# Kernel optimization log

Hardware: AMD Instinct MI355X
Metric: run time of the kernel (lower is better)

Reference implementation:

```python
import jax, jax.numpy as jnp
import numpy as np

B, S = 128, 400
EMB, ENC, DEC = 128, 1024, 300
VOCAB, MAX_OOV = 50000, 50


def setup_inputs() -> dict:
    key = jax.random.key(0)
    ks = jax.random.split(key, 16)
    s = 0.05
    return {
        "embedded": jax.random.normal(ks[0], (B, EMB), jnp.float32),
        "enc_output": jax.random.normal(ks[1], (B, S, ENC), jnp.float32),
        "h1": jax.random.normal(ks[2], (B, DEC), jnp.float32),
        "pad_mask": jnp.zeros((B, S), jnp.bool_),
        "max_n_oov": MAX_OOV,
        "source_WORD_encoding_extended": jax.random.randint(ks[3], (B, S), 0, VOCAB + MAX_OOV),
        # parameters
        "W_attn1": jax.random.normal(ks[4], (ENC, DEC), jnp.float32) * s,
        "W_attn2": jax.random.normal(ks[5], (ENC, DEC), jnp.float32) * s,
        "W_ih": jax.random.normal(ks[6], (3 * DEC, EMB + ENC), jnp.float32) * s,
        "W_hh": jax.random.normal(ks[7], (3 * DEC, DEC), jnp.float32) * s,
        "b_ih": jax.random.normal(ks[8], (3 * DEC,), jnp.float32) * s,
        "b_hh": jax.random.normal(ks[9], (3 * DEC,), jnp.float32) * s,
        "W_out": jax.random.normal(ks[10], (VOCAB, ENC + DEC), jnp.float32) * s,
        "b_out": jax.random.normal(ks[11], (VOCAB,), jnp.float32) * s,
        "W_p": jax.random.normal(ks[12], (1, ENC + DEC), jnp.float32) * s,
        "b_p": jax.random.normal(ks[13], (1,), jnp.float32) * s,
    }


def _additive_attn(h, enc_output, W, pad_mask):
    # h: [B, DEC], enc_output: [B, S, ENC], W: [ENC, DEC]
    e = jnp.einsum('bse,ed->bsd', enc_output, W)
    scores = jnp.einsum('bd,bsd->bs', h, e)
    scores = jnp.where(pad_mask, -jnp.inf, scores)
    return jax.nn.softmax(scores, axis=1)  # [B, S]


def _gru_cell(x, h, W_ih, W_hh, b_ih, b_hh):
    gx = x @ W_ih.T + b_ih  # [B, 3*DEC]
    gh = h @ W_hh.T + b_hh
    xr, xz, xn = jnp.split(gx, 3, axis=1)
    hr, hz, hn = jnp.split(gh, 3, axis=1)
    r = jax.nn.sigmoid(xr + hr)
    z = jax.nn.sigmoid(xz + hz)
    n = jnp.tanh(xn + r * hn)
    return (1.0 - z) * n + z * h


def reference(embedded, enc_output, h1, pad_mask, max_n_oov,
              source_WORD_encoding_extended, W_attn1, W_attn2,
              W_ih, W_hh, b_ih, b_hh, W_out, b_out, W_p, b_p):
    a = _additive_attn(h1, enc_output, W_attn1, pad_mask)
    weighted = jnp.einsum('bs,bse->be', a, enc_output)
    rnn_input = jnp.concatenate([embedded, weighted], axis=1)
    h_new = _gru_cell(rnn_input, h1, W_ih, W_hh, b_ih, b_hh)

    a2 = _additive_attn(h_new, enc_output, W_attn2, pad_mask)
    weighted2 = jnp.einsum('bs,bse->be', a2, enc_output)
    hw = jnp.concatenate([h_new, weighted2], axis=1)  # [B, DEC+ENC]

    p_vocab = jax.nn.softmax(hw @ W_out.T + b_out, axis=1)  # [B, VOCAB]
    p_gen = jax.nn.sigmoid(hw @ W_p.T + b_p)  # [B, 1]

    bsz = p_vocab.shape[0]
    ext_zeros = jnp.zeros((bsz, max_n_oov), p_vocab.dtype)
    p_out = p_gen * jnp.concatenate([p_vocab, ext_zeros], axis=1)
    rows = jnp.arange(bsz)[:, None]
    p_out = p_out.at[rows, source_WORD_encoding_extended].add((1.0 - p_gen) * a2)
    return p_out, h_new
```

## Files before the change

### kernel.cpp

```cpp
#include <hip/hip_runtime.h>
#include <stdint.h>

constexpr int B_     = 128;
constexpr int S_     = 400;
constexpr int EMB_   = 128;
constexpr int ENC_   = 1024;
constexpr int DEC_   = 300;
constexpr int VOCAB_ = 50000;
constexpr int OOV_   = 50;
constexpr int OUTW_  = VOCAB_ + OOV_;
constexpr int KHW_   = ENC_ + DEC_;
constexpr int KHWP_  = 1344;
constexpr int G3_    = 3 * DEC_;
constexpr int KIN_   = EMB_ + ENC_;
constexpr int CHK_   = 192;
constexpr int ALDS_STRIDE_ = 200;
constexpr int PSTRIDE_ = 1028;

typedef __attribute__((ext_vector_type(4))) float f32x4;
typedef __attribute__((ext_vector_type(8))) short short8;

__device__ __forceinline__ float dot4(float4 a, float4 b) {
  return a.x * b.x + a.y * b.y + a.z * b.z + a.w * b.w;
}

__device__ __forceinline__ short f2bf(float f) {
  uint32_t u = __builtin_bit_cast(uint32_t, f);
  u += 0x7fffu + ((u >> 16) & 1u);
  return (short)(u >> 16);
}

__global__ __launch_bounds__(256) void k_compute_v(const float* __restrict__ W,
                                                   const float* __restrict__ h,
                                                   float* __restrict__ v) {
  int b = blockIdx.x;
  __shared__ __align__(16) float hs[DEC_];
  for (int d = threadIdx.x; d < DEC_; d += 256) hs[d] = h[b * DEC_ + d];
  __syncthreads();
  for (int e = threadIdx.x; e < ENC_; e += 256) {
    const float4* w4 = (const float4*)(W + (size_t)e * DEC_);
    const float4* h4 = (const float4*)hs;
    float acc = 0.f;
    #pragma unroll 5
    for (int d = 0; d < DEC_ / 4; ++d) acc += dot4(w4[d], h4[d]);
    v[b * ENC_ + e] = acc;
  }
}

__global__ __launch_bounds__(256) void k_attn_pass(const float* __restrict__ enc,
                                                   const float* __restrict__ v,
                                                   float* __restrict__ scores,
                                                   float* __restrict__ part, int nsplit) {
  int b = blockIdx.x, split = blockIdx.y;
  int wave = threadIdx.x >> 6, lane = threadIdx.x & 63;
  float4 vr[4];
  #pragma unroll
  for (int c = 0; c < 4; ++c) vr[c] = *(const float4*)(v + b * ENC_ + c * 256 + lane * 4);
  float m = -INFINITY, l = 0.f;
  float4 wa[4];
  #pragma unroll
  for (int c = 0; c < 4; ++c) wa[c] = make_float4(0.f, 0.f, 0.f, 0.f);
  int rows = S_ / nsplit, s0 = split * rows;
  for (int s = s0 + wave; s < s0 + rows; s += 4) {
    const float* er = enc + ((size_t)b * S_ + s) * ENC_;
    float4 e4[4];
    #pragma unroll
    for (int c = 0; c < 4; ++c) e4[c] = *(const float4*)(er + c * 256 + lane * 4);
    float p = 0.f;
    #pragma unroll
    for (int c = 0; c < 4; ++c) p += dot4(e4[c], vr[c]);
    #pragma unroll
    for (int off = 32; off; off >>= 1) p += __shfl_xor(p, off);
    if (lane == 0) scores[b * S_ + s] = p;
    float nm = fmaxf(m, p);
    float sc = __expf(m - nm);
    float pe = __expf(p - nm);
    l = l * sc + pe;
    #pragma unroll
    for (int c = 0; c < 4; ++c) {
      wa[c].x = wa[c].x * sc + pe * e4[c].x;
      wa[c].y = wa[c].y * sc + pe * e4[c].y;
      wa[c].z = wa[c].z * sc + pe * e4[c].z;
      wa[c].w = wa[c].w * sc + pe * e4[c].w;
    }
    m = nm;
  }
  float* pp = part + ((size_t)b * (nsplit * 4) + split * 4 + wave) * PSTRIDE_;
  #pragma unroll
  for (int c = 0; c < 4; ++c) *(float4*)(pp + c * 256 + lane * 4) = wa[c];
  if (lane == 0) { pp[1024] = m; pp[1025] = l; }
}

__global__ __launch_bounds__(256) void k_attn_merge(const float* __restrict__ part, int P,
                                                    float* __restrict__ wout, int wstride,
                                                    int woff, float* __restrict__ ml) {
  int b = blockIdx.x, tid = threadIdx.x;
  const float* pb = part + (size_t)b * P * PSTRIDE_;
  __shared__ float scl[32];
  __shared__ float Ls;
  if (tid == 0) {
    float M = -INFINITY;
    for (int p = 0; p < P; ++p) M = fmaxf(M, pb[p * PSTRIDE_ + 1024]);
    float L = 0.f;
    for (int p = 0; p < P; ++p) {
      float lp = pb[p * PSTRIDE_ + 1025];
      float e = (lp > 0.f) ? __expf(pb[p * PSTRIDE_ + 1024] - M) : 0.f;
      scl[p] = e;
      L += lp * e;
    }
    Ls = L;
    if (ml) { ml[b * 2] = M; ml[b * 2 + 1] = L; }
  }
  __syncthreads();
  float invL = 1.f / Ls;
  for (int e = tid; e < ENC_; e += 256) {
    float acc = 0.f;
    for (int p = 0; p < P; ++p) acc += scl[p] * pb[p * PSTRIDE_ + e];
    wout[(size_t)b * wstride + woff + e] = acc * invL;
  }
}

__global__ __launch_bounds__(256) void k_gates(const float* __restrict__ emb,
                                               const float* __restrict__ wgt,
                                               const float* __restrict__ h1,
                                               const float* __restrict__ W_ih,
                                               const float* __restrict__ W_hh,
                                               const float* __restrict__ b_ih,
                                               const float* __restrict__ b_hh,
                                               float* __restrict__ gx, float* __restrict__ gh) {
  int idx = blockIdx.x * 256 + threadIdx.x;
  int b = idx & (B_ - 1);
  int g = idx >> 7;
  if (g >= G3_) return;
  const float4* wr = (const float4*)(W_ih + (size_t)g * KIN_);
  const float4* xe = (const float4*)(emb + b * EMB_);
  const float4* xw = (const float4*)(wgt + b * ENC_);
  float accx = b_ih[g];
  #pragma unroll 8
  for (int k = 0; k < EMB_ / 4; ++k) accx += dot4(wr[k], xe[k]);
  #pragma unroll 8
  for (int k = 0; k < ENC_ / 4; ++k) accx += dot4(wr[EMB_ / 4 + k], xw[k]);
  const float4* wh = (const float4*)(W_hh + (size_t)g * DEC_);
  const float4* xh = (const float4*)(h1 + b * DEC_);
  float acch = b_hh[g];
  #pragma unroll 5
  for (int k = 0; k < DEC_ / 4; ++k) acch += dot4(wh[k], xh[k]);
  gx[g * B_ + b] = accx;
  gh[g * B_ + b] = acch;
}

__global__ __launch_bounds__(256) void k_gru_combine(const float* __restrict__ gx,
                                                     const float* __restrict__ gh,
                                                     const float* __restrict__ h1,
                                                     float* __restrict__ hn,
                                                     float* __restrict__ hw,
                                                     float* __restrict__ outh) {
  int j = blockIdx.x * 256 + threadIdx.x;
  int b = blockIdx.y;
  if (j >= DEC_) return;
  float xr = gx[j * B_ + b], xz = gx[(j + DEC_) * B_ + b], xn = gx[(j + 2 * DEC_) * B_ + b];
  float hr = gh[j * B_ + b], hz = gh[(j + DEC_) * B_ + b], hnn = gh[(j + 2 * DEC_) * B_ + b];
  float r = 1.f / (1.f + __expf(-(xr + hr)));
  float z = 1.f / (1.f + __expf(-(xz + hz)));
  float n = tanhf(xn + r * hnn);
  float h = (1.f - z) * n + z * h1[b * DEC_ + j];
  hn[b * DEC_ + j] = h;
  hw[(size_t)b * KHW_ + j] = h;
  outh[b * DEC_ + j] = h;
}

__global__ __launch_bounds__(256) void k_pgen_cast(const float* __restrict__ hw,
                                                   const float* __restrict__ W_p,
                                                   const float* __restrict__ b_p,
                                                   float* __restrict__ pg,
                                                   short* __restrict__ hwb) {
  int b = blockIdx.x, t = threadIdx.x;
  __shared__ float red[256];
  const float* row = hw + (size_t)b * KHW_;
  float acc = 0.f;
  for (int k = t; k < KHW_; k += 256) acc += row[k] * W_p[k];
  red[t] = acc;
  __syncthreads();
  for (int st = 128; st > 0; st >>= 1) {
    if (t < st) red[t] += red[t + st];
    __syncthreads();
  }
  if (t == 0) pg[b] = 1.f / (1.f + __expf(-(red[0] + b_p[0])));
  for (int k = t; k < KHWP_; k += 256)
    hwb[(size_t)b * KHWP_ + k] = (k < KHW_) ? f2bf(row[k]) : (short)0;
}

__global__ __launch_bounds__(256) void k_outproj(const short* __restrict__ A,
                                                 const float* __restrict__ Wo,
                                                 const float* __restrict__ bo,
                                                 float* __restrict__ out) {
  __shared__ __align__(16) short A_lds[B_ * ALDS_STRIDE_];
  int tid = threadIdx.x;
  int wave = tid >> 6, lane = tid & 63;
  int r16 = lane & 15, kg = lane >> 4;
  int vcol = blockIdx.x * 64 + wave * 16 + r16;
  int vload = vcol < VOCAB_ ? vcol : VOCAB_ - 1;
  const float* brow = Wo + (size_t)vload * KHW_ + kg * 8;
  f32x4 acc[8];
  #pragma unroll
  for (int mi = 0; mi < 8; ++mi) acc[mi] = (f32x4){0.f, 0.f, 0.f, 0.f};

  short8 ar[12];
  float4 br[2][12];
  float  tl[8];

  #pragma unroll
  for (int i = 0; i < 12; ++i) {
    int g = tid + i * 256, row = g / 24, c8 = g % 24;
    ar[i] = *(const short8*)(A + (size_t)row * KHWP_ + c8 * 8);
  }
  #pragma unroll
  for (int s = 0; s < 6; ++s) {
    br[0][2 * s]     = *(const float4*)(brow + s * 32);
    br[0][2 * s + 1] = *(const float4*)(brow + s * 32 + 4);
  }

  #pragma unroll
  for (int c = 0; c < 7; ++c) {
    __syncthreads();
    #pragma unroll
    for (int i = 0; i < 12; ++i) {
      int g = tid + i * 256, row = g / 24, c8 = g % 24;
      *(short8*)(&A_lds[row * ALDS_STRIDE_ + c8 * 8]) = ar[i];
    }
    if (c < 6) {
      #pragma unroll
      for (int i = 0; i < 12; ++i) {
        int g = tid + i * 256, row = g / 24, c8 = g % 24;
        ar[i] = *(const short8*)(A + (size_t)row * KHWP_ + (c + 1) * CHK_ + c8 * 8);
      }
      if (c + 1 < 6) {
        #pragma unroll
        for (int s = 0; s < 6; ++s) {
          br[(c + 1) & 1][2 * s]     = *(const float4*)(brow + (c + 1) * CHK_ + s * 32);
          br[(c + 1) & 1][2 * s + 1] = *(const float4*)(brow + (c + 1) * CHK_ + s * 32 + 4);
        }
      } else {
        #pragma unroll
        for (int s = 0; s < 5; ++s) {
          br[0][2 * s]     = *(const float4*)(brow + 6 * CHK_ + s * 32);
          br[0][2 * s + 1] = *(const float4*)(brow + 6 * CHK_ + s * 32 + 4);
        }
        #pragma unroll
        for (int j = 0; j < 8; ++j)
          tl[j] = (kg * 8 + j < KHW_ - 1312) ? brow[1312 + j] : 0.f;
      }
    }
    __syncthreads();
    #pragma unroll
    for (int s = 0; s < 6; ++s) {
      short8 bf;
      if (c == 6 && s == 5) {
        #pragma unroll
        for (int j = 0; j < 8; ++j) bf[j] = f2bf(tl[j]);
      } else {
        float4 b0 = br[c & 1][2 * s], b1 = br[c & 1][2 * s + 1];
        bf[0] = f2bf(b0.x); bf[1] = f2bf(b0.y); bf[2] = f2bf(b0.z); bf[3] = f2bf(b0.w);
        bf[4] = f2bf(b1.x); bf[5] = f2bf(b1.y); bf[6] = f2bf(b1.z); bf[7] = f2bf(b1.w);
      }
      #pragma unroll
      for (int mi = 0; mi < 8; ++mi) {
        short8 af = *(const short8*)(&A_lds[(mi * 16 + r16) * ALDS_STRIDE_ + s * 32 + kg * 8]);
        acc[mi] = __builtin_amdgcn_mfma_f32_16x16x32_bf16(af, bf, acc[mi], 0, 0, 0);
      }
    }
  }

  if (vcol < VOCAB_) {
    float bias = bo[vcol];
    #pragma unroll
    for (int mi = 0; mi < 8; ++mi) {
      #pragma unroll
      for (int j = 0; j < 4; ++j) {
        out[(size_t)(mi * 16 + kg * 4 + j) * OUTW_ + vcol] = acc[mi][j] + bias;
      }
    }
  }
}

__global__ __launch_bounds__(256) void k_vocab_softmax(float* __restrict__ out,
                                                       const float* __restrict__ pg,
                                                       const int* __restrict__ src,
                                                       const float* __restrict__ scores,
                                                       const float* __restrict__ ml2) {
  int b = blockIdx.x, t = threadIdx.x;
  float* row = out + (size_t)b * OUTW_;
  __shared__ float red[256];
  float mx = -INFINITY;
  for (int v = t; v < VOCAB_; v += 256) mx = fmaxf(mx, row[v]);
  red[t] = mx;
  __syncthreads();
  for (int st = 128; st > 0; st >>= 1) {
    if (t < st) red[t] = fmaxf(red[t], red[t + st]);
    __syncthreads();
  }
  float M = red[0];
  __syncthreads();
  float sm = 0.f;
  for (int v = t; v < VOCAB_; v += 256) sm += __expf(row[v] - M);
  red[t] = sm;
  __syncthreads();
  for (int st = 128; st > 0; st >>= 1) {
    if (t < st) red[t] += red[t + st];
    __syncthreads();
  }
  float p = pg[b];
  float scale = p / red[0];
  for (int v = t; v < OUTW_; v += 256) {
    row[v] = (v < VOCAB_) ? scale * __expf(row[v] - M) : 0.f;
  }
  __syncthreads();
  float M2 = ml2[b * 2], L2 = ml2[b * 2 + 1];
  float q = (1.f - p) / L2;
  for (int s = t; s < S_; s += 256) {
    float val = q * __expf(scores[b * S_ + s] - M2);
    atomicAdd(row + src[b * S_ + s], val);
  }
}

extern "C" void kernel_launch(void* const* d_in, const int* in_sizes, int n_in,
                              void* d_out, int out_size, void* d_ws, size_t ws_size,
                              hipStream_t stream) {
  const float* embedded = (const float*)d_in[0];
  const float* enc      = (const float*)d_in[1];
  const float* h1       = (const float*)d_in[2];
  const int*   src      = (const int*)d_in[5];
  const float* W1       = (const float*)d_in[6];
  const float* W2       = (const float*)d_in[7];
  const float* W_ih     = (const float*)d_in[8];
  const float* W_hh     = (const float*)d_in[9];
  const float* b_ih     = (const float*)d_in[10];
  const float* b_hh     = (const float*)d_in[11];
  const float* W_out    = (const float*)d_in[12];
  const float* b_out    = (const float*)d_in[13];
  const float* W_p      = (const float*)d_in[14];
  const float* b_p      = (const float*)d_in[15];
  float* out = (float*)d_out;
  float* ws  = (float*)d_ws;

  size_t off = 0;
  float* v_ws    = ws + off; off += (size_t)B_ * ENC_;
  float* w1_ws   = ws + off; off += (size_t)B_ * ENC_;
  float* gx_ws   = ws + off; off += (size_t)G3_ * B_;
  float* gh_ws   = ws + off; off += (size_t)G3_ * B_;
  float* hn_ws   = ws + off; off += (size_t)B_ * DEC_;
  float* hw_ws   = ws + off; off += (size_t)B_ * KHW_;
  float* sc_ws   = ws + off; off += (size_t)B_ * S_;
  float* ml2_ws  = ws + off; off += 256;
  float* pg_ws   = ws + off; off += 128;
  short* hwb_ws  = (short*)(ws + off); off += (size_t)B_ * KHWP_ / 2;
  float* part_ws = ws + off;

  int NS = 4;
  if ((off + (size_t)B_ * NS * 4 * PSTRIDE_) * 4 > ws_size) NS = 1;

  k_compute_v<<<B_, 256, 0, stream>>>(W1, h1, v_ws);
  k_attn_pass<<<dim3(B_, NS), 256, 0, stream>>>(enc, v_ws, sc_ws, part_ws, NS);
  k_attn_merge<<<B_, 256, 0, stream>>>(part_ws, NS * 4, w1_ws, ENC_, 0, nullptr);
  k_gates<<<(G3_ * B_) / 256, 256, 0, stream>>>(embedded, w1_ws, h1, W_ih, W_hh, b_ih, b_hh,
                                                gx_ws, gh_ws);
  k_gru_combine<<<dim3(2, B_), 256, 0, stream>>>(gx_ws, gh_ws, h1, hn_ws, hw_ws,
                                                 out + (size_t)B_ * OUTW_);
  k_compute_v<<<B_, 256, 0, stream>>>(W2, hn_ws, v_ws);
  k_attn_pass<<<dim3(B_, NS), 256, 0, stream>>>(enc, v_ws, sc_ws, part_ws, NS);
  k_attn_merge<<<B_, 256, 0, stream>>>(part_ws, NS * 4, hw_ws, KHW_, DEC_, ml2_ws);
  k_pgen_cast<<<B_, 256, 0, stream>>>(hw_ws, W_p, b_p, pg_ws, hwb_ws);
  k_outproj<<<(VOCAB_ + 63) / 64, 256, 0, stream>>>(hwb_ws, W_out, b_out, out);
  k_vocab_softmax<<<B_, 256, 0, stream>>>(out, pg_ws, src, sc_ws, ml2_ws);
}
```

Before: 477.5 us.

## Fuse vocab softmax stats into outproj, fold pgen into merges, unroll attention

The output projection now computes per-tile row max and sum-exp partials, and a new split kernel merges them and normalises the vocab logits in a single pass. This replaces the old three-pass per-row softmax that ran on only one block per batch row. The p_gen dot product and the bf16 cast are folded into the GRU combine and the second attention merge, which removes the k_pgen_cast kernel and the fp32 hw buffer. The attention pass now processes two rows per iteration and uses up to 8 splits for more parallelism, at the cost of extra workspace and an atomic accumulation for p_gen.

```diff
diff --git a/kernel.cpp b/kernel.cpp
--- a/kernel.cpp
+++ b/kernel.cpp
@@ -16,6 +16,7 @@
 constexpr int CHK_   = 192;
 constexpr int ALDS_STRIDE_ = 200;
 constexpr int PSTRIDE_ = 1028;
+constexpr int NTILE_ = 782;
 
 typedef __attribute__((ext_vector_type(4))) float f32x4;
 typedef __attribute__((ext_vector_type(8))) short short8;
@@ -60,8 +61,41 @@
   float4 wa[4];
   #pragma unroll
   for (int c = 0; c < 4; ++c) wa[c] = make_float4(0.f, 0.f, 0.f, 0.f);
-  int rows = S_ / nsplit, s0 = split * rows;
-  for (int s = s0 + wave; s < s0 + rows; s += 4) {
+  int rows = S_ / nsplit, s0 = split * rows, s_end = s0 + rows;
+  int s = s0 + wave;
+  for (; s + 4 < s_end; s += 8) {
+    const float* era = enc + ((size_t)b * S_ + s) * ENC_;
+    const float* erb = enc + ((size_t)b * S_ + s + 4) * ENC_;
+    float4 e4a[4], e4b[4];
+    #pragma unroll
+    for (int c = 0; c < 4; ++c) {
+      e4a[c] = *(const float4*)(era + c * 256 + lane * 4);
+      e4b[c] = *(const float4*)(erb + c * 256 + lane * 4);
+    }
+    float pa = 0.f, pb = 0.f;
+    #pragma unroll
+    for (int c = 0; c < 4; ++c) { pa += dot4(e4a[c], vr[c]); pb += dot4(e4b[c], vr[c]); }
+    #pragma unroll
+    for (int off = 32; off; off >>= 1) {
+      pa += __shfl_xor(pa, off);
+      pb += __shfl_xor(pb, off);
+    }
+    if (lane == 0) { scores[b * S_ + s] = pa; scores[b * S_ + s + 4] = pb; }
+    float nm = fmaxf(m, fmaxf(pa, pb));
+    float sc = __expf(m - nm);
+    float ea = __expf(pa - nm);
+    float eb = __expf(pb - nm);
+    l = l * sc + ea + eb;
+    #pragma unroll
+    for (int c = 0; c < 4; ++c) {
+      wa[c].x = wa[c].x * sc + ea * e4a[c].x + eb * e4b[c].x;
+      wa[c].y = wa[c].y * sc + ea * e4a[c].y + eb * e4b[c].y;
+      wa[c].z = wa[c].z * sc + ea * e4a[c].z + eb * e4b[c].z;
+      wa[c].w = wa[c].w * sc + ea * e4a[c].w + eb * e4b[c].w;
+    }
+    m = nm;
+  }
+  if (s < s_end) {
     const float* er = enc + ((size_t)b * S_ + s) * ENC_;
     float4 e4[4];
     #pragma unroll
@@ -73,8 +107,7 @@
     for (int off = 32; off; off >>= 1) p += __shfl_xor(p, off);
     if (lane == 0) scores[b * S_ + s] = p;
     float nm = fmaxf(m, p);
-    float sc = __expf(m - nm);
-    float pe = __expf(p - nm);
+    float sc = __expf(m - nm), pe = __expf(p - nm);
     l = l * sc + pe;
     #pragma unroll
     for (int c = 0; c < 4; ++c) {
@@ -91,9 +124,8 @@
   if (lane == 0) { pp[1024] = m; pp[1025] = l; }
 }
 
-__global__ __launch_bounds__(256) void k_attn_merge(const float* __restrict__ part, int P,
-                                                    float* __restrict__ wout, int wstride,
-                                                    int woff, float* __restrict__ ml) {
+__global__ __launch_bounds__(256) void k_attn_merge1(const float* __restrict__ part, int P,
+                                                     float* __restrict__ wout) {
   int b = blockIdx.x, tid = threadIdx.x;
   const float* pb = part + (size_t)b * P * PSTRIDE_;
   __shared__ float scl[32];
@@ -109,15 +141,59 @@
       L += lp * e;
     }
     Ls = L;
-    if (ml) { ml[b * 2] = M; ml[b * 2 + 1] = L; }
   }
   __syncthreads();
   float invL = 1.f / Ls;
   for (int e = tid; e < ENC_; e += 256) {
     float acc = 0.f;
     for (int p = 0; p < P; ++p) acc += scl[p] * pb[p * PSTRIDE_ + e];
-    wout[(size_t)b * wstride + woff + e] = acc * invL;
-  }
+    wout[(size_t)b * ENC_ + e] = acc * invL;
+  }
+}
+
+__global__ __launch_bounds__(256) void k_attn_merge2(const float* __restrict__ part, int P,
+                                                     short* __restrict__ hwb,
+                                                     float* __restrict__ ml,
+                                                     const float* __restrict__ W_p,
+                                                     const float* __restrict__ b_p,
+                                                     const float* __restrict__ pg_acc,
+                                                     float* __restrict__ pg) {
+  int b = blockIdx.x, tid = threadIdx.x;
+  const float* pb = part + (size_t)b * P * PSTRIDE_;
+  __shared__ float scl[32];
+  __shared__ float Ls;
+  __shared__ float red[256];
+  if (tid == 0) {
+    float M = -INFINITY;
+    for (int p = 0; p < P; ++p) M = fmaxf(M, pb[p * PSTRIDE_ + 1024]);
+    float L = 0.f;
+    for (int p = 0; p < P; ++p) {
+      float lp = pb[p * PSTRIDE_ + 1025];
+      float e = (lp > 0.f) ? __expf(pb[p * PSTRIDE_ + 1024] - M) : 0.f;
+      scl[p] = e;
+      L += lp * e;
+    }
+    Ls = L;
+    ml[b * 2] = M; ml[b * 2 + 1] = L;
+  }
+  __syncthreads();
+  float invL = 1.f / Ls;
+  float pacc = 0.f;
+  for (int e = tid; e < ENC_; e += 256) {
+    float acc = 0.f;
+    for (int p = 0; p < P; ++p) acc += scl[p] * pb[p * PSTRIDE_ + e];
+    float w = acc * invL;
+    hwb[(size_t)b * KHWP_ + DEC_ + e] = f2bf(w);
+    pacc += w * W_p[DEC_ + e];
+  }
+  if (tid < KHWP_ - KHW_) hwb[(size_t)b * KHWP_ + KHW_ + tid] = 0;
+  red[tid] = pacc;
+  __syncthreads();
+  for (int st = 128; st > 0; st >>= 1) {
+    if (tid < st) red[tid] += red[tid + st];
+    __syncthreads();
+  }
+  if (tid == 0) pg[b] = 1.f / (1.f + __expf(-(red[0] + pg_acc[b] + b_p[0])));
 }
 
 __global__ __launch_bounds__(256) void k_gates(const float* __restrict__ emb,
@@ -127,8 +203,10 @@
                                                const float* __restrict__ W_hh,
                                                const float* __restrict__ b_ih,
                                                const float* __restrict__ b_hh,
-                                               float* __restrict__ gx, float* __restrict__ gh) {
+                                               float* __restrict__ gx, float* __restrict__ gh,
+                                               float* __restrict__ pg_acc) {
   int idx = blockIdx.x * 256 + threadIdx.x;
+  if (idx < B_) pg_acc[idx] = 0.f;
   int b = idx & (B_ - 1);
   int g = idx >> 7;
   if (g >= G3_) return;
@@ -153,48 +231,42 @@
                                                      const float* __restrict__ gh,
                                                      const float* __restrict__ h1,
                                                      float* __restrict__ hn,
-                                                     float* __restrict__ hw,
-                                                     float* __restrict__ outh) {
+                                                     short* __restrict__ hwb,
+                                                     float* __restrict__ outh,
+                                                     const float* __restrict__ W_p,
+                                                     float* __restrict__ pg_acc) {
   int j = blockIdx.x * 256 + threadIdx.x;
   int b = blockIdx.y;
-  if (j >= DEC_) return;
-  float xr = gx[j * B_ + b], xz = gx[(j + DEC_) * B_ + b], xn = gx[(j + 2 * DEC_) * B_ + b];
-  float hr = gh[j * B_ + b], hz = gh[(j + DEC_) * B_ + b], hnn = gh[(j + 2 * DEC_) * B_ + b];
-  float r = 1.f / (1.f + __expf(-(xr + hr)));
-  float z = 1.f / (1.f + __expf(-(xz + hz)));
-  float n = tanhf(xn + r * hnn);
-  float h = (1.f - z) * n + z * h1[b * DEC_ + j];
-  hn[b * DEC_ + j] = h;
-  hw[(size_t)b * KHW_ + j] = h;
-  outh[b * DEC_ + j] = h;
-}
-
-__global__ __launch_bounds__(256) void k_pgen_cast(const float* __restrict__ hw,
-                                                   const float* __restrict__ W_p,
-                                                   const float* __restrict__ b_p,
-                                                   float* __restrict__ pg,
-                                                   short* __restrict__ hwb) {
-  int b = blockIdx.x, t = threadIdx.x;
   __shared__ float red[256];
-  const float* row = hw + (size_t)b * KHW_;
-  float acc = 0.f;
-  for (int k = t; k < KHW_; k += 256) acc += row[k] * W_p[k];
-  red[t] = acc;
+  float pp = 0.f;
+  if (j < DEC_) {
+    float xr = gx[j * B_ + b], xz = gx[(j + DEC_) * B_ + b], xn = gx[(j + 2 * DEC_) * B_ + b];
+    float hr = gh[j * B_ + b], hz = gh[(j + DEC_) * B_ + b], hnn = gh[(j + 2 * DEC_) * B_ + b];
+    float r = 1.f / (1.f + __expf(-(xr + hr)));
+    float z = 1.f / (1.f + __expf(-(xz + hz)));
+    float n = tanhf(xn + r * hnn);
+    float h = (1.f - z) * n + z * h1[b * DEC_ + j];
+    hn[b * DEC_ + j] = h;
+    hwb[(size_t)b * KHWP_ + j] = f2bf(h);
+    outh[b * DEC_ + j] = h;
+    pp = h * W_p[j];
+  }
+  red[threadIdx.x] = pp;
   __syncthreads();
   for (int st = 128; st > 0; st >>= 1) {
-    if (t < st) red[t] += red[t + st];
+    if (threadIdx.x < st) red[threadIdx.x] += red[threadIdx.x + st];
     __syncthreads();
   }
-  if (t == 0) pg[b] = 1.f / (1.f + __expf(-(red[0] + b_p[0])));
-  for (int k = t; k < KHWP_; k += 256)
-    hwb[(size_t)b * KHWP_ + k] = (k < KHW_) ? f2bf(row[k]) : (short)0;
+  if (threadIdx.x == 0) atomicAdd(pg_acc + b, red[0]);
 }
 
 __global__ __launch_bounds__(256) void k_outproj(const short* __restrict__ A,
                                                  const float* __restrict__ Wo,
                                                  const float* __restrict__ bo,
-                                                 float* __restrict__ out) {
+                                                 float* __restrict__ out,
+                                                 float* __restrict__ pml) {
   __shared__ __align__(16) short A_lds[B_ * ALDS_STRIDE_];
+  __shared__ float wml[4][B_][2];
   int tid = threadIdx.x;
   int wave = tid >> 6, lane = tid & 63;
   int r16 = lane & 15, kg = lane >> 4;
@@ -271,52 +343,88 @@
     }
   }
 
-  if (vcol < VOCAB_) {
-    float bias = bo[vcol];
-    #pragma unroll
-    for (int mi = 0; mi < 8; ++mi) {
+  bool valid = vcol < VOCAB_;
+  float biasv = bo[vload];
+  #pragma unroll
+  for (int mi = 0; mi < 8; ++mi) {
+    #pragma unroll
+    for (int j = 0; j < 4; ++j) {
+      float lv = valid ? acc[mi][j] + biasv : -INFINITY;
+      if (valid) out[(size_t)(mi * 16 + kg * 4 + j) * OUTW_ + vcol] = lv;
+      float mr = lv;
       #pragma unroll
-      for (int j = 0; j < 4; ++j) {
-        out[(size_t)(mi * 16 + kg * 4 + j) * OUTW_ + vcol] = acc[mi][j] + bias;
+      for (int msk = 1; msk < 16; msk <<= 1) mr = fmaxf(mr, __shfl_xor(mr, msk));
+      float se = valid ? __expf(lv - mr) : 0.f;
+      #pragma unroll
+      for (int msk = 1; msk < 16; msk <<= 1) se += __shfl_xor(se, msk);
+      if (r16 == 0) {
+        wml[wave][mi * 16 + kg * 4 + j][0] = mr;
+        wml[wave][mi * 16 + kg * 4 + j][1] = se;
       }
     }
   }
-}
-
-__global__ __launch_bounds__(256) void k_vocab_softmax(float* __restrict__ out,
-                                                       const float* __restrict__ pg,
-                                                       const int* __restrict__ src,
-                                                       const float* __restrict__ scores,
-                                                       const float* __restrict__ ml2) {
+  __syncthreads();
+  if (tid < B_) {
+    float M = -INFINITY;
+    #pragma unroll
+    for (int w = 0; w < 4; ++w) M = fmaxf(M, wml[w][tid][0]);
+    float L = 0.f;
+    #pragma unroll
+    for (int w = 0; w < 4; ++w) {
+      float lw = wml[w][tid][1];
+      if (lw > 0.f) L += lw * __expf(wml[w][tid][0] - M);
+    }
+    pml[((size_t)blockIdx.x * B_ + tid) * 2]     = M;
+    pml[((size_t)blockIdx.x * B_ + tid) * 2 + 1] = L;
+  }
+}
+
+__global__ __launch_bounds__(256) void k_vfinal(float* __restrict__ out,
+                                                const float* __restrict__ pml,
+                                                const float* __restrict__ pg,
+                                                float* __restrict__ mlv) {
+  int bq = blockIdx.x, b = blockIdx.y, t = threadIdx.x;
+  __shared__ float rm[256], rl[256];
+  float lm = -INFINITY, ll = 0.f;
+  for (int tile = t; tile < NTILE_; tile += 256) {
+    float m = pml[((size_t)tile * B_ + b) * 2];
+    float l = pml[((size_t)tile * B_ + b) * 2 + 1];
+    float M = fmaxf(lm, m);
+    float nl = 0.f;
+    if (ll > 0.f) nl += ll * __expf(lm - M);
+    if (l > 0.f) nl += l * __expf(m - M);
+    lm = M; ll = nl;
+  }
+  rm[t] = lm; rl[t] = ll;
+  __syncthreads();
+  for (int st = 128; st > 0; st >>= 1) {
+    if (t < st) {
+      float m1 = rm[t], l1 = rl[t], m2 = rm[t + st], l2 = rl[t + st];
+      float M = fmaxf(m1, m2);
+      float L = (l1 > 0.f ? l1 * __expf(m1 - M) : 0.f) + (l2 > 0.f ? l2 * __expf(m2 - M) : 0.f);
+      rm[t] = M; rl[t] = L;
+    }
+    __syncthreads();
+  }
+  float M = rm[0], L = rl[0];
+  float scale = pg[b] / L;
+  float* row = out + (size_t)b * OUTW_;
+  int lo = bq * 12513;
+  int hi = min(lo + 12513, OUTW_);
+  for (int v = lo + t; v < hi; v += 256)
+    row[v] = (v < VOCAB_) ? scale * __expf(row[v] - M) : 0.f;
+  if (bq == 0 && t == 0) { mlv[b * 2] = M; mlv[b * 2 + 1] = L; }
+}
+
+__global__ __launch_bounds__(256) void k_scatter2(float* __restrict__ out,
+                                                  const int* __restrict__ src,
+                                                  const float* __restrict__ scores,
+                                                  const float* __restrict__ ml2,
+                                                  const float* __restrict__ pg) {
   int b = blockIdx.x, t = threadIdx.x;
+  float M2 = ml2[b * 2], L2 = ml2[b * 2 + 1];
+  float q = (1.f - pg[b]) / L2;
   float* row = out + (size_t)b * OUTW_;
-  __shared__ float red[256];
-  float mx = -INFINITY;
-  for (int v = t; v < VOCAB_; v += 256) mx = fmaxf(mx, row[v]);
-  red[t] = mx;
-  __syncthreads();
-  for (int st = 128; st > 0; st >>= 1) {
-    if (t < st) red[t] = fmaxf(red[t], red[t + st]);
-    __syncthreads();
-  }
-  float M = red[0];
-  __syncthreads();
-  float sm = 0.f;
-  for (int v = t; v < VOCAB_; v += 256) sm += __expf(row[v] - M);
-  red[t] = sm;
-  __syncthreads();
-  for (int st = 128; st > 0; st >>= 1) {
-    if (t < st) red[t] += red[t + st];
-    __syncthreads();
-  }
-  float p = pg[b];
-  float scale = p / red[0];
-  for (int v = t; v < OUTW_; v += 256) {
-    row[v] = (v < VOCAB_) ? scale * __expf(row[v] - M) : 0.f;
-  }
-  __syncthreads();
-  float M2 = ml2[b * 2], L2 = ml2[b * 2 + 1];
-  float q = (1.f - p) / L2;
   for (int s = t; s < S_; s += 256) {
     float val = q * __expf(scores[b * S_ + s] - M2);
     atomicAdd(row + src[b * S_ + s], val);
@@ -349,27 +457,30 @@
   float* gx_ws   = ws + off; off += (size_t)G3_ * B_;
   float* gh_ws   = ws + off; off += (size_t)G3_ * B_;
   float* hn_ws   = ws + off; off += (size_t)B_ * DEC_;
-  float* hw_ws   = ws + off; off += (size_t)B_ * KHW_;
   float* sc_ws   = ws + off; off += (size_t)B_ * S_;
   float* ml2_ws  = ws + off; off += 256;
   float* pg_ws   = ws + off; off += 128;
+  float* pga_ws  = ws + off; off += 128;
+  float* mlv_ws  = ws + off; off += 256;
+  float* pml_ws  = ws + off; off += (size_t)NTILE_ * B_ * 2;
   short* hwb_ws  = (short*)(ws + off); off += (size_t)B_ * KHWP_ / 2;
   float* part_ws = ws + off;
 
-  int NS = 4;
-  if ((off + (size_t)B_ * NS * 4 * PSTRIDE_) * 4 > ws_size) NS = 1;
+  int NS = 8;
+  while (NS > 1 && (off + (size_t)B_ * NS * 4 * PSTRIDE_) * 4 > ws_size) NS >>= 1;
 
   k_compute_v<<<B_, 256, 0, stream>>>(W1, h1, v_ws);
   k_attn_pass<<<dim3(B_, NS), 256, 0, stream>>>(enc, v_ws, sc_ws, part_ws, NS);
-  k_attn_merge<<<B_, 256, 0, stream>>>(part_ws, NS * 4, w1_ws, ENC_, 0, nullptr);
+  k_attn_merge1<<<B_, 256, 0, stream>>>(part_ws, NS * 4, w1_ws);
   k_gates<<<(G3_ * B_) / 256, 256, 0, stream>>>(embedded, w1_ws, h1, W_ih, W_hh, b_ih, b_hh,
-                                                gx_ws, gh_ws);
-  k_gru_combine<<<dim3(2, B_), 256, 0, stream>>>(gx_ws, gh_ws, h1, hn_ws, hw_ws,
-                                                 out + (size_t)B_ * OUTW_);
+                                                gx_ws, gh_ws, pga_ws);
+  k_gru_combine<<<dim3(2, B_), 256, 0, stream>>>(gx_ws, gh_ws, h1, hn_ws, hwb_ws,
+                                                 out + (size_t)B_ * OUTW_, W_p, pga_ws);
   k_compute_v<<<B_, 256, 0, stream>>>(W2, hn_ws, v_ws);
   k_attn_pass<<<dim3(B_, NS), 256, 0, stream>>>(enc, v_ws, sc_ws, part_ws, NS);
-  k_attn_merge<<<B_, 256, 0, stream>>>(part_ws, NS * 4, hw_ws, KHW_, DEC_, ml2_ws);
-  k_pgen_cast<<<B_, 256, 0, stream>>>(hw_ws, W_p, b_p, pg_ws, hwb_ws);
-  k_outproj<<<(VOCAB_ + 63) / 64, 256, 0, stream>>>(hwb_ws, W_out, b_out, out);
-  k_vocab_softmax<<<B_, 256, 0, stream>>>(out, pg_ws, src, sc_ws, ml2_ws);
-}
+  k_attn_merge2<<<B_, 256, 0, stream>>>(part_ws, NS * 4, hwb_ws, ml2_ws, W_p, b_p,
+                                        pga_ws, pg_ws);
+  k_outproj<<<NTILE_, 256, 0, stream>>>(hwb_ws, W_out, b_out, out, pml_ws);
+  k_vfinal<<<dim3(4, B_), 256, 0, stream>>>(out, pml_ws, pg_ws, mlv_ws);
+  k_scatter2<<<B_, 256, 0, stream>>>(out, src, sc_ws, ml2_ws, pg_ws);
+}
```

Result: slower. 516.4 us (+8.2%).
